# Kernel tuning notes

Hardware: AMD Instinct MI355X
Metric: run time of the kernel (lower is better)

The kernel has to match this reference:

```python
import jax, jax.numpy as jnp
import numpy as np

HEADS = 16
DIM_HEAD = 64
QUERY_DIM = 1024
INNER_DIM = HEADS * DIM_HEAD  # 1024
SCALE = DIM_HEAD ** (-0.5)


def setup_inputs() -> dict:
    key = jax.random.key(0)
    ks = jax.random.split(key, 6)
    B, S = 4, 2048
    hidden_states = jax.random.normal(ks[0], (B, S, QUERY_DIM), dtype=jnp.float32)
    # Linear weights stored as [in, out] for x @ W convention
    init = 1.0 / np.sqrt(QUERY_DIM)
    Wq = jax.random.uniform(ks[1], (QUERY_DIM, INNER_DIM), jnp.float32, -init, init)
    Wk = jax.random.uniform(ks[2], (QUERY_DIM, INNER_DIM), jnp.float32, -init, init)
    Wv = jax.random.uniform(ks[3], (QUERY_DIM, INNER_DIM), jnp.float32, -init, init)
    Wo = jax.random.uniform(ks[4], (INNER_DIM, QUERY_DIM), jnp.float32, -init, init)
    bo = jax.random.uniform(ks[5], (QUERY_DIM,), jnp.float32, -init, init)
    return {"hidden_states": hidden_states, "Wq": Wq, "Wk": Wk, "Wv": Wv, "Wo": Wo, "bo": bo}


def reference(hidden_states, Wq, Wk, Wv, Wo, bo):
    B, S, _ = hidden_states.shape
    # Projections
    q = hidden_states @ Wq  # [B,S,inner]
    k = hidden_states @ Wk
    v = hidden_states @ Wv
    # [B, H, S, D]
    q = q.reshape(B, S, HEADS, DIM_HEAD).transpose(0, 2, 1, 3)
    k = k.reshape(B, S, HEADS, DIM_HEAD).transpose(0, 2, 1, 3)
    v = v.reshape(B, S, HEADS, DIM_HEAD).transpose(0, 2, 1, 3)
    # Attention scores and softmax (scale after matmul, as in source)
    scores = jnp.einsum('bhqd,bhkd->bhqk', q, k) * SCALE
    attn = jax.nn.softmax(scores, axis=-1)
    out = jnp.einsum('bhqk,bhkd->bhqd', attn, v)  # [B,H,S,D]
    out = out.transpose(0, 2, 1, 3).reshape(B, S, INNER_DIM)
    return out @ Wo + bo
```

## Files before the change

kernel.cpp:

```cpp
#include <hip/hip_runtime.h>
#include <stdint.h>

typedef short v8s __attribute__((ext_vector_type(8)));
typedef float v4f __attribute__((ext_vector_type(4)));
typedef unsigned int u32;
typedef unsigned short us;

#define LOG2E 1.44269504088896340736f

__device__ __forceinline__ u32 f2u(float x) {
  union { float f; u32 u; } t; t.f = x; return t.u;
}

__device__ __forceinline__ unsigned short bfr(float x) {
  u32 u = f2u(x);
  u32 r = u + 0x7FFFu + ((u >> 16) & 1u);
  return (unsigned short)(r >> 16);
}

__device__ __forceinline__ u32 pk2(float a, float b) {
  return __builtin_amdgcn_perm(f2u(b) + 0x8000u, f2u(a) + 0x8000u, 0x07060302u);
}

__device__ __forceinline__ void async16(const void* g, void* l) {
  __builtin_amdgcn_global_load_lds(
      (const __attribute__((address_space(1))) u32*)g,
      (__attribute__((address_space(3))) u32*)l, 16, 0, 0);
}

#define MFMA_K32(A, B, C) __builtin_amdgcn_mfma_f32_16x16x32_bf16((A), (B), (C), 0, 0, 0)

__global__ __launch_bounds__(256)
void prologue_kernel(const float4* __restrict__ Hs, ushort4* __restrict__ Hb,
                     const float* __restrict__ W0, const float* __restrict__ W1,
                     const float* __restrict__ W2, const float* __restrict__ W3,
                     us* __restrict__ O0, us* __restrict__ O1,
                     us* __restrict__ O2, us* __restrict__ O3) {
  __shared__ float tile[32][33];
  const int bid = blockIdx.x;
  if (bid < 8192) {
    int i = bid * 256 + threadIdx.x;
    float4 v = Hs[i];
    ushort4 o;
    o.x = bfr(v.x); o.y = bfr(v.y); o.z = bfr(v.z); o.w = bfr(v.w);
    Hb[i] = o;
  } else {
    const int b = bid - 8192;
    const int z = b >> 10;
    const int ti = b & 1023;
    const float* in = (z == 0) ? W0 : (z == 1) ? W1 : (z == 2) ? W2 : W3;
    us* out = (z == 0) ? O0 : (z == 1) ? O1 : (z == 2) ? O2 : O3;
    const float scale = (z == 0) ? 0.125f * LOG2E : 1.0f;
    const int N = 1024;
    int n0 = (ti & 31) * 32, k0 = (ti >> 5) * 32;
    int tx = threadIdx.x & 31, ty = threadIdx.x >> 5;
#pragma unroll
    for (int j = 0; j < 32; j += 8)
      tile[ty + j][tx] = in[(size_t)(k0 + ty + j) * N + n0 + tx];
    __syncthreads();
#pragma unroll
    for (int j = 0; j < 32; j += 8)
      out[(size_t)(n0 + ty + j) * 1024 + k0 + tx] = bfr(tile[tx][ty + j] * scale);
  }
}

template <int MODE>
__global__ __launch_bounds__(512, 2)
void gemm3_kernel(const us* __restrict__ A, const us* __restrict__ Bt,
                  us* __restrict__ dQ, us* __restrict__ dK, us* __restrict__ dV,
                  float* __restrict__ outF, const float* __restrict__ bias) {
  __shared__ __align__(16) us sm[73728];
  us* const AsB = sm;
  us* const BsB = sm + 3 * 8192;

  const int tid = threadIdx.x;
  const int wid = tid >> 6;
  const int lane = tid & 63;
  const int quad = lane >> 4;
  const int l16 = lane & 15;
  const int tile_m = blockIdx.y * 128;
  const int tile_n = blockIdx.x * 256;
  const bool vpath = (MODE == 3) && (tile_n >= 2048);

  const int srow = tid >> 3;
  const int sc = tid & 7;
  const int scg = sc ^ (srow & 7);

  const us* const GA = A + (size_t)(tile_m + srow) * 1024 + scg * 8;
  const us* const GB = Bt + (size_t)(tile_n + srow) * 1024 + scg * 8;
  us* const LA = AsB + srow * 64 + sc * 8;
  us* const LB = BsB + srow * 64 + sc * 8;

  auto ISSUE = [&](int j, int b) {
    const us* ga = GA + j * 64;
    us* la = LA + b * 8192;
#pragma unroll
    for (int it = 0; it < 2; ++it)
      async16(ga + it * 64 * 1024, la + it * 64 * 64);
    const us* gb = GB + j * 64;
    us* lb = LB + b * 16384;
#pragma unroll
    for (int it = 0; it < 4; ++it)
      async16(gb + it * 64 * 1024, lb + it * 64 * 64);
  };

  v4f zero = {0.f, 0.f, 0.f, 0.f};
  v4f acc[4][4];
#pragma unroll
  for (int i = 0; i < 4; ++i)
#pragma unroll
    for (int j = 0; j < 4; ++j) acc[i][j] = zero;

  const int wm = (wid >> 2) * 64;
  const int wn = (wid & 3) * 64;

  ISSUE(0, 0);
  ISSUE(1, 1);

  int bt = 0;
#pragma unroll 1
  for (int t = 0; t < 16; ++t) {
    if (t < 15)
      asm volatile("s_waitcnt vmcnt(6)" ::: "memory");
    else
      asm volatile("s_waitcnt vmcnt(0)" ::: "memory");
    __builtin_amdgcn_s_barrier();
    asm volatile("" ::: "memory");

    if (t + 2 < 16) {
      int b2 = bt + 2;
      if (b2 >= 3) b2 -= 3;
      ISSUE(t + 2, b2);
    }

    const us* As = AsB + bt * 8192;
    const us* Bs = BsB + bt * 16384;
#pragma unroll
    for (int ks = 0; ks < 2; ++ks) {
      v8s a[4], b[4];
#pragma unroll
      for (int i = 0; i < 4; ++i) {
        int row = wm + i * 16 + l16;
        a[i] = *(const v8s*)&As[row * 64 + (((ks * 4 + quad) ^ (row & 7)) * 8)];
      }
#pragma unroll
      for (int j = 0; j < 4; ++j) {
        int row = wn + j * 16 + l16;
        b[j] = *(const v8s*)&Bs[row * 64 + (((ks * 4 + quad) ^ (row & 7)) * 8)];
      }
      __builtin_amdgcn_s_setprio(1);
      if (vpath) {
#pragma unroll
        for (int i = 0; i < 4; ++i)
#pragma unroll
          for (int j = 0; j < 4; ++j)
            acc[i][j] = MFMA_K32(a[i], b[j], acc[i][j]);
      } else {
#pragma unroll
        for (int i = 0; i < 4; ++i)
#pragma unroll
          for (int j = 0; j < 4; ++j)
            acc[i][j] = MFMA_K32(b[j], a[i], acc[i][j]);
      }
      __builtin_amdgcn_s_setprio(0);
    }
    if (++bt >= 3) bt = 0;
  }

  if (MODE == 2) {
#pragma unroll
    for (int i = 0; i < 4; ++i) {
      int row = tile_m + wm + i * 16 + l16;
#pragma unroll
      for (int j = 0; j < 4; ++j) {
        int col = tile_n + wn + j * 16 + quad * 4;
        float4 bv = *(const float4*)&bias[col];
        float4 o;
        o.x = acc[i][j][0] + bv.x; o.y = acc[i][j][1] + bv.y;
        o.z = acc[i][j][2] + bv.z; o.w = acc[i][j][3] + bv.w;
        *(float4*)&outF[(size_t)row * 1024 + col] = o;
      }
    }
  } else if (!vpath) {
    us* base = (tile_n < 1024) ? dQ : dK;
    const int coln = tile_n & 1023;
#pragma unroll
    for (int i = 0; i < 4; ++i) {
      int row = tile_m + wm + i * 16 + l16;
      int b_ = row >> 11, s_ = row & 2047;
#pragma unroll
      for (int j = 0; j < 4; ++j) {
        int col = coln + wn + j * 16 + quad * 4;
        int h = (col >> 6) & 15, d = col & 63;
        uint2 pk = make_uint2(pk2(acc[i][j][0], acc[i][j][1]), pk2(acc[i][j][2], acc[i][j][3]));
        *(uint2*)&base[((size_t)(b_ * 16 + h) * 2048 + s_) * 64 + d] = pk;
      }
    }
  } else {
    __syncthreads();
    const int vn = tile_n - 2048;
#pragma unroll
    for (int i = 0; i < 4; ++i) {
      int sp = wm + (i >> 1) * 32 + quad * 8 + (i & 1) * 4;
#pragma unroll
      for (int j = 0; j < 4; ++j) {
        int col = wn + j * 16 + l16;
        uint2 pk = make_uint2(pk2(acc[i][j][0], acc[i][j][1]), pk2(acc[i][j][2], acc[i][j][3]));
        *(uint2*)&sm[col * 132 + sp] = pk;
      }
    }
    __syncthreads();
    const int b_ = tile_m >> 11;
    const int sbase = tile_m & 2047;
#pragma unroll
    for (int it = 0; it < 8; ++it) {
      int u = it * 512 + tid;
      int col = u >> 4, sp = (u & 15) * 8;
      v8s val = *(const v8s*)&sm[col * 132 + sp];
      int colg = vn + col;
      int h = (colg >> 6) & 15, d = colg & 63;
      *(v8s*)&dV[((size_t)(b_ * 16 + h) * 64 + d) * 2048 + sbase + sp] = val;
    }
  }
}

__global__ __launch_bounds__(256, 2)
void flash_kernel(const us* __restrict__ Q, const us* __restrict__ K,
                  const us* __restrict__ Vt, us* __restrict__ O) {
  __shared__ __align__(16) us sm[32768];

  const int tid = threadIdx.x;
  const int wid = tid >> 6;
  const int lane = tid & 63;
  const int quad = lane >> 4;
  const int l16 = lane & 15;
  const int id = blockIdx.x;
  const int bh = id & 63;
  const int q0 = (id >> 6) * 256;
  const int wq = wid * 64;
  const us* Qp = Q + (size_t)bh * (2048 * 64);
  const us* Kp = K + (size_t)bh * (2048 * 64);
  const us* Vp = Vt + (size_t)bh * (64 * 2048);

  v8s qB[4][2];
#pragma unroll
  for (int mi = 0; mi < 4; ++mi)
#pragma unroll
    for (int ks = 0; ks < 2; ++ks)
      qB[mi][ks] = *(const v8s*)&Qp[(size_t)(q0 + wq + mi * 16 + l16) * 64 + ks * 32 + quad * 8];

  v4f zero = {0.f, 0.f, 0.f, 0.f};
  v4f o[4][4];
#pragma unroll
  for (int i = 0; i < 4; ++i)
#pragma unroll
    for (int mi = 0; mi < 4; ++mi) o[i][mi] = zero;
  v4f l_acc[4] = {zero, zero, zero, zero};
  const us one_bf = 0x3F80;
  const v8s ones = {(short)one_bf, (short)one_bf, (short)one_bf, (short)one_bf,
                    (short)one_bf, (short)one_bf, (short)one_bf, (short)one_bf};

  auto STAGE = [&](int kv0, int p) {
    us* Ks = sm + p * 16384;
    us* Vts = Ks + 8192;
    {
      int r0 = wid * 32 + (lane >> 3);
      int c = lane & 7;
#pragma unroll
      for (int it = 0; it < 4; ++it) {
        int rr = r0 + it * 8;
        int cg = c ^ (rr & 7);
        async16(Kp + (size_t)(kv0 + rr) * 64 + cg * 8, &Ks[rr * 64 + c * 8]);
      }
    }
    {
      int d0 = wid * 16 + (lane >> 4);
      int c = lane & 15;
#pragma unroll
      for (int it = 0; it < 4; ++it) {
        int dd = d0 + it * 4;
        int cg = c ^ (dd & 15);
        async16(Vp + (size_t)dd * 2048 + kv0 + cg * 8, &Vts[dd * 128 + c * 8]);
      }
    }
  };

  STAGE(0, 0);
  int buf = 0;
#pragma unroll 1
  for (int t = 0; t < 16; ++t) {
    asm volatile("s_waitcnt vmcnt(0)" ::: "memory");
    __builtin_amdgcn_s_barrier();
    asm volatile("" ::: "memory");
    if (t < 15) STAGE((t + 1) * 128, buf ^ 1);

    const us* Ks = sm + buf * 16384;
    const us* Vts = Ks + 8192;

#pragma unroll
    for (int hf = 0; hf < 2; ++hf) {
      v4f sT[4][4];
#pragma unroll
      for (int m = 0; m < 4; ++m)
#pragma unroll
        for (int mi = 0; mi < 4; ++mi) sT[m][mi] = zero;
#pragma unroll
      for (int ks = 0; ks < 2; ++ks) {
        v8s kA[4];
#pragma unroll
        for (int m = 0; m < 4; ++m) {
          int kvr = hf * 64 + m * 16 + l16;
          int cc = (ks * 4 + quad) ^ (l16 & 7);
          kA[m] = *(const v8s*)&Ks[kvr * 64 + cc * 8];
        }
#pragma unroll
        for (int m = 0; m < 4; ++m)
#pragma unroll
          for (int mi = 0; mi < 4; ++mi)
            sT[m][mi] = MFMA_K32(kA[m], qB[mi][ks], sT[m][mi]);
      }

#pragma unroll
      for (int cp = 0; cp < 2; ++cp) {
        v8s bp[4];
#pragma unroll
        for (int mi = 0; mi < 4; ++mi) {
          union { u32 w[4]; v8s s; } u;
#pragma unroll
          for (int dm = 0; dm < 2; ++dm) {
            int m = cp * 2 + dm;
            float p0 = __builtin_amdgcn_exp2f(sT[m][mi][0]);
            float p1 = __builtin_amdgcn_exp2f(sT[m][mi][1]);
            float p2 = __builtin_amdgcn_exp2f(sT[m][mi][2]);
            float p3 = __builtin_amdgcn_exp2f(sT[m][mi][3]);
            u.w[dm * 2] = pk2(p0, p1);
            u.w[dm * 2 + 1] = pk2(p2, p3);
          }
          bp[mi] = u.s;
          l_acc[mi] = MFMA_K32(ones, bp[mi], l_acc[mi]);
        }
#pragma unroll
        for (int i = 0; i < 4; ++i) {
          int d = i * 16 + l16;
          int cc = (hf * 8 + cp * 4 + quad) ^ (d & 15);
          v8s vt = *(const v8s*)&Vts[d * 128 + cc * 8];
#pragma unroll
          for (int mi = 0; mi < 4; ++mi)
            o[i][mi] = MFMA_K32(vt, bp[mi], o[i][mi]);
        }
      }
    }
    buf ^= 1;
  }

  float invl[4];
#pragma unroll
  for (int mi = 0; mi < 4; ++mi) invl[mi] = 1.0f / l_acc[mi][0];

  __syncthreads();
#pragma unroll
  for (int mi = 0; mi < 4; ++mi) {
    int q = wq + mi * 16 + l16;
#pragma unroll
    for (int i = 0; i < 4; ++i)
#pragma unroll
      for (int rp = 0; rp < 4; rp += 2) {
        int d = i * 16 + quad * 4 + rp;
        u32 pk = pk2(o[i][mi][rp] * invl[mi], o[i][mi][rp + 1] * invl[mi]);
        *(u32*)&sm[q * 64 + ((d >> 3) ^ (q & 7)) * 8 + (d & 7)] = pk;
      }
  }
  __syncthreads();
  const int b_ = bh >> 4, h_ = bh & 15;
#pragma unroll
  for (int it = 0; it < 8; ++it) {
    int u = it * 256 + tid;
    int row = u >> 3, ch = u & 7;
    v8s val = *(const v8s*)&sm[row * 64 + (ch ^ (row & 7)) * 8];
    *(v8s*)&O[((size_t)(b_ * 2048 + q0 + row)) * 1024 + h_ * 64 + ch * 8] = val;
  }
}

extern "C" void kernel_launch(void* const* d_in, const int* in_sizes, int n_in,
                              void* d_out, int out_size, void* d_ws, size_t ws_size,
                              hipStream_t stream) {
  const float* Hs = (const float*)d_in[0];
  const float* Wq = (const float*)d_in[1];
  const float* Wk = (const float*)d_in[2];
  const float* Wv = (const float*)d_in[3];
  const float* Wo = (const float*)d_in[4];
  const float* bo = (const float*)d_in[5];
  float* out = (float*)d_out;
  char* ws = (char*)d_ws;
  const size_t MiB = 1ull << 20;
  us* Hb  = (us*)(ws);
  us* Wqt = (us*)(ws + 16 * MiB);
  us* Wkt = (us*)(ws + 18 * MiB);
  us* Wvt = (us*)(ws + 20 * MiB);
  us* Wot = (us*)(ws + 22 * MiB);
  us* Qb  = (us*)(ws + 24 * MiB);
  us* Kb  = (us*)(ws + 40 * MiB);
  us* Vtb = (us*)(ws + 56 * MiB);
  us* Ob  = Hb;
  (void)Wkt; (void)Wvt;

  prologue_kernel<<<12288, 256, 0, stream>>>((const float4*)Hs, (ushort4*)Hb,
                                             Wq, Wk, Wv, Wo, Wqt, Wkt, Wvt, Wot);
  gemm3_kernel<3><<<dim3(12, 64), 512, 0, stream>>>(Hb, Wqt, Qb, Kb, Vtb, nullptr, nullptr);
  flash_kernel<<<512, 256, 0, stream>>>(Qb, Kb, Vtb, Ob);
  gemm3_kernel<2><<<dim3(4, 64), 512, 0, stream>>>(Ob, Wot, nullptr, nullptr, nullptr, out, bo);
}
```

Before: 259.4 us.

## Fuse fp32-to-bf16 activation cast into QKV GEMM A-tile loads

Removes the separate pass that converts hidden_states to bf16. The QKV GEMM now reads fp32 A tiles straight from global memory into registers, packs them to bf16 and writes them to LDS one stage ahead, while the B tiles keep using async global-to-LDS loads. This drops one full-activation write and read round trip. In exchange the A loads are register-staged, and each tile fetches twice the bytes from global memory. Launch bounds also change to 4 waves per SIMD, which may limit registers and cause spills.

```diff
diff --git a/kernel.cpp b/kernel.cpp
--- a/kernel.cpp
+++ b/kernel.cpp
@@ -30,45 +30,30 @@
 
 #define MFMA_K32(A, B, C) __builtin_amdgcn_mfma_f32_16x16x32_bf16((A), (B), (C), 0, 0, 0)
 
-__global__ __launch_bounds__(256)
-void prologue_kernel(const float4* __restrict__ Hs, ushort4* __restrict__ Hb,
-                     const float* __restrict__ W0, const float* __restrict__ W1,
-                     const float* __restrict__ W2, const float* __restrict__ W3,
-                     us* __restrict__ O0, us* __restrict__ O1,
-                     us* __restrict__ O2, us* __restrict__ O3) {
+__global__ void transpose_cast4_kernel(const float* __restrict__ W0, const float* __restrict__ W1,
+                                       const float* __restrict__ W2, const float* __restrict__ W3,
+                                       us* __restrict__ O0, us* __restrict__ O1,
+                                       us* __restrict__ O2, us* __restrict__ O3) {
   __shared__ float tile[32][33];
-  const int bid = blockIdx.x;
-  if (bid < 8192) {
-    int i = bid * 256 + threadIdx.x;
-    float4 v = Hs[i];
-    ushort4 o;
-    o.x = bfr(v.x); o.y = bfr(v.y); o.z = bfr(v.z); o.w = bfr(v.w);
-    Hb[i] = o;
-  } else {
-    const int b = bid - 8192;
-    const int z = b >> 10;
-    const int ti = b & 1023;
-    const float* in = (z == 0) ? W0 : (z == 1) ? W1 : (z == 2) ? W2 : W3;
-    us* out = (z == 0) ? O0 : (z == 1) ? O1 : (z == 2) ? O2 : O3;
-    const float scale = (z == 0) ? 0.125f * LOG2E : 1.0f;
-    const int N = 1024;
-    int n0 = (ti & 31) * 32, k0 = (ti >> 5) * 32;
-    int tx = threadIdx.x & 31, ty = threadIdx.x >> 5;
-#pragma unroll
-    for (int j = 0; j < 32; j += 8)
-      tile[ty + j][tx] = in[(size_t)(k0 + ty + j) * N + n0 + tx];
-    __syncthreads();
-#pragma unroll
-    for (int j = 0; j < 32; j += 8)
-      out[(size_t)(n0 + ty + j) * 1024 + k0 + tx] = bfr(tile[tx][ty + j] * scale);
-  }
-}
-
-template <int MODE>
-__global__ __launch_bounds__(512, 2)
-void gemm3_kernel(const us* __restrict__ A, const us* __restrict__ Bt,
-                  us* __restrict__ dQ, us* __restrict__ dK, us* __restrict__ dV,
-                  float* __restrict__ outF, const float* __restrict__ bias) {
+  const int z = blockIdx.z;
+  const float* in = (z == 0) ? W0 : (z == 1) ? W1 : (z == 2) ? W2 : W3;
+  us* out = (z == 0) ? O0 : (z == 1) ? O1 : (z == 2) ? O2 : O3;
+  const float scale = (z == 0) ? 0.125f * LOG2E : 1.0f;
+  const int N = 1024;
+  int n0 = blockIdx.x * 32, k0 = blockIdx.y * 32;
+  int tx = threadIdx.x, ty = threadIdx.y;
+#pragma unroll
+  for (int j = 0; j < 32; j += 8)
+    tile[ty + j][tx] = in[(size_t)(k0 + ty + j) * N + n0 + tx];
+  __syncthreads();
+#pragma unroll
+  for (int j = 0; j < 32; j += 8)
+    out[(size_t)(n0 + ty + j) * 1024 + k0 + tx] = bfr(tile[tx][ty + j] * scale);
+}
+
+__global__ __launch_bounds__(512, 4)
+void gemm_qkv_kernel(const float* __restrict__ A, const us* __restrict__ Bt,
+                     us* __restrict__ dQ, us* __restrict__ dK, us* __restrict__ dV) {
   __shared__ __align__(16) us sm[73728];
   us* const AsB = sm;
   us* const BsB = sm + 3 * 8192;
@@ -80,7 +65,167 @@
   const int l16 = lane & 15;
   const int tile_m = blockIdx.y * 128;
   const int tile_n = blockIdx.x * 256;
-  const bool vpath = (MODE == 3) && (tile_n >= 2048);
+  const bool vpath = (tile_n >= 2048);
+
+  const int srow = tid >> 3;
+  const int sc = tid & 7;
+  const int scg = sc ^ (srow & 7);
+
+  const float* const GA = A + (size_t)(tile_m + srow) * 1024 + scg * 8;
+  const us* const GB = Bt + (size_t)(tile_n + srow) * 1024 + scg * 8;
+  us* const LA = AsB + srow * 64 + sc * 8;
+  us* const LB = BsB + srow * 64 + sc * 8;
+
+  float4 aR[4];
+
+  auto LOAD_A = [&](int j) {
+    const float4* p0 = (const float4*)(GA + j * 64);
+    const float4* p1 = (const float4*)(GA + j * 64 + (size_t)64 * 1024);
+    aR[0] = p0[0]; aR[1] = p0[1];
+    aR[2] = p1[0]; aR[3] = p1[1];
+  };
+  auto WRITE_A = [&](int b) {
+    uint4 w0, w1;
+    w0.x = pk2(aR[0].x, aR[0].y); w0.y = pk2(aR[0].z, aR[0].w);
+    w0.z = pk2(aR[1].x, aR[1].y); w0.w = pk2(aR[1].z, aR[1].w);
+    w1.x = pk2(aR[2].x, aR[2].y); w1.y = pk2(aR[2].z, aR[2].w);
+    w1.z = pk2(aR[3].x, aR[3].y); w1.w = pk2(aR[3].z, aR[3].w);
+    *(uint4*)(LA + b * 8192) = w0;
+    *(uint4*)(LA + b * 8192 + 64 * 64) = w1;
+  };
+  auto ISSUE_B = [&](int j, int b) {
+    const us* gb = GB + j * 64;
+    us* lb = LB + b * 16384;
+#pragma unroll
+    for (int it = 0; it < 4; ++it)
+      async16(gb + it * 64 * 1024, lb + it * 64 * 64);
+  };
+
+  v4f zero = {0.f, 0.f, 0.f, 0.f};
+  v4f acc[4][4];
+#pragma unroll
+  for (int i = 0; i < 4; ++i)
+#pragma unroll
+    for (int j = 0; j < 4; ++j) acc[i][j] = zero;
+
+  const int wm = (wid >> 2) * 64;
+  const int wn = (wid & 3) * 64;
+
+  LOAD_A(0);
+  ISSUE_B(0, 0);
+  WRITE_A(0);
+  LOAD_A(1);
+  ISSUE_B(1, 1);
+
+  int bt = 0;
+#pragma unroll 1
+  for (int t = 0; t < 16; ++t) {
+    if (t < 15)
+      asm volatile("s_waitcnt vmcnt(8)" ::: "memory");
+    else
+      asm volatile("s_waitcnt vmcnt(0)" ::: "memory");
+    asm volatile("s_waitcnt lgkmcnt(0)" ::: "memory");
+    __builtin_amdgcn_s_barrier();
+    asm volatile("" ::: "memory");
+
+    {
+      int b1 = bt + 1; if (b1 >= 3) b1 -= 3;
+      int b2 = bt + 2; if (b2 >= 3) b2 -= 3;
+      if (t + 1 < 16) WRITE_A(b1);
+      if (t + 2 < 16) { LOAD_A(t + 2); ISSUE_B(t + 2, b2); }
+    }
+
+    const us* As = AsB + bt * 8192;
+    const us* Bs = BsB + bt * 16384;
+#pragma unroll
+    for (int ks = 0; ks < 2; ++ks) {
+      v8s a[4], b[4];
+#pragma unroll
+      for (int i = 0; i < 4; ++i) {
+        int row = wm + i * 16 + l16;
+        a[i] = *(const v8s*)&As[row * 64 + (((ks * 4 + quad) ^ (row & 7)) * 8)];
+      }
+#pragma unroll
+      for (int j = 0; j < 4; ++j) {
+        int row = wn + j * 16 + l16;
+        b[j] = *(const v8s*)&Bs[row * 64 + (((ks * 4 + quad) ^ (row & 7)) * 8)];
+      }
+      __builtin_amdgcn_s_setprio(1);
+      if (vpath) {
+#pragma unroll
+        for (int i = 0; i < 4; ++i)
+#pragma unroll
+          for (int j = 0; j < 4; ++j)
+            acc[i][j] = MFMA_K32(a[i], b[j], acc[i][j]);
+      } else {
+#pragma unroll
+        for (int i = 0; i < 4; ++i)
+#pragma unroll
+          for (int j = 0; j < 4; ++j)
+            acc[i][j] = MFMA_K32(b[j], a[i], acc[i][j]);
+      }
+      __builtin_amdgcn_s_setprio(0);
+    }
+    if (++bt >= 3) bt = 0;
+  }
+
+  if (!vpath) {
+    us* base = (tile_n < 1024) ? dQ : dK;
+    const int coln = tile_n & 1023;
+#pragma unroll
+    for (int i = 0; i < 4; ++i) {
+      int row = tile_m + wm + i * 16 + l16;
+      int b_ = row >> 11, s_ = row & 2047;
+#pragma unroll
+      for (int j = 0; j < 4; ++j) {
+        int col = coln + wn + j * 16 + quad * 4;
+        int h = (col >> 6) & 15, d = col & 63;
+        uint2 pk = make_uint2(pk2(acc[i][j][0], acc[i][j][1]), pk2(acc[i][j][2], acc[i][j][3]));
+        *(uint2*)&base[((size_t)(b_ * 16 + h) * 2048 + s_) * 64 + d] = pk;
+      }
+    }
+  } else {
+    __syncthreads();
+    const int vn = tile_n - 2048;
+#pragma unroll
+    for (int i = 0; i < 4; ++i) {
+      int sp = wm + (i >> 1) * 32 + quad * 8 + (i & 1) * 4;
+#pragma unroll
+      for (int j = 0; j < 4; ++j) {
+        int col = wn + j * 16 + l16;
+        uint2 pk = make_uint2(pk2(acc[i][j][0], acc[i][j][1]), pk2(acc[i][j][2], acc[i][j][3]));
+        *(uint2*)&sm[col * 132 + sp] = pk;
+      }
+    }
+    __syncthreads();
+    const int b_ = tile_m >> 11;
+    const int sbase = tile_m & 2047;
+#pragma unroll
+    for (int it = 0; it < 8; ++it) {
+      int u = it * 512 + tid;
+      int col = u >> 4, sp = (u & 15) * 8;
+      v8s val = *(const v8s*)&sm[col * 132 + sp];
+      int colg = vn + col;
+      int h = (colg >> 6) & 15, d = colg & 63;
+      *(v8s*)&dV[((size_t)(b_ * 16 + h) * 64 + d) * 2048 + sbase + sp] = val;
+    }
+  }
+}
+
+__global__ __launch_bounds__(512, 2)
+void gemm_out_kernel(const us* __restrict__ A, const us* __restrict__ Bt,
+                     float* __restrict__ outF, const float* __restrict__ bias) {
+  __shared__ __align__(16) us sm[73728];
+  us* const AsB = sm;
+  us* const BsB = sm + 3 * 8192;
+
+  const int tid = threadIdx.x;
+  const int wid = tid >> 6;
+  const int lane = tid & 63;
+  const int quad = lane >> 4;
+  const int l16 = lane & 15;
+  const int tile_m = blockIdx.y * 128;
+  const int tile_n = blockIdx.x * 256;
 
   const int srow = tid >> 3;
   const int sc = tid & 7;
@@ -149,77 +294,27 @@
         b[j] = *(const v8s*)&Bs[row * 64 + (((ks * 4 + quad) ^ (row & 7)) * 8)];
       }
       __builtin_amdgcn_s_setprio(1);
-      if (vpath) {
-#pragma unroll
-        for (int i = 0; i < 4; ++i)
-#pragma unroll
-          for (int j = 0; j < 4; ++j)
-            acc[i][j] = MFMA_K32(a[i], b[j], acc[i][j]);
-      } else {
-#pragma unroll
-        for (int i = 0; i < 4; ++i)
-#pragma unroll
-          for (int j = 0; j < 4; ++j)
-            acc[i][j] = MFMA_K32(b[j], a[i], acc[i][j]);
-      }
+#pragma unroll
+      for (int i = 0; i < 4; ++i)
+#pragma unroll
+        for (int j = 0; j < 4; ++j)
+          acc[i][j] = MFMA_K32(b[j], a[i], acc[i][j]);
       __builtin_amdgcn_s_setprio(0);
     }
     if (++bt >= 3) bt = 0;
   }
 
-  if (MODE == 2) {
-#pragma unroll
-    for (int i = 0; i < 4; ++i) {
-      int row = tile_m + wm + i * 16 + l16;
-#pragma unroll
-      for (int j = 0; j < 4; ++j) {
-        int col = tile_n + wn + j * 16 + quad * 4;
-        float4 bv = *(const float4*)&bias[col];
-        float4 o;
-        o.x = acc[i][j][0] + bv.x; o.y = acc[i][j][1] + bv.y;
-        o.z = acc[i][j][2] + bv.z; o.w = acc[i][j][3] + bv.w;
-        *(float4*)&outF[(size_t)row * 1024 + col] = o;
-      }
-    }
-  } else if (!vpath) {
-    us* base = (tile_n < 1024) ? dQ : dK;
-    const int coln = tile_n & 1023;
-#pragma unroll
-    for (int i = 0; i < 4; ++i) {
-      int row = tile_m + wm + i * 16 + l16;
-      int b_ = row >> 11, s_ = row & 2047;
-#pragma unroll
-      for (int j = 0; j < 4; ++j) {
-        int col = coln + wn + j * 16 + quad * 4;
-        int h = (col >> 6) & 15, d = col & 63;
-        uint2 pk = make_uint2(pk2(acc[i][j][0], acc[i][j][1]), pk2(acc[i][j][2], acc[i][j][3]));
-        *(uint2*)&base[((size_t)(b_ * 16 + h) * 2048 + s_) * 64 + d] = pk;
-      }
-    }
-  } else {
-    __syncthreads();
-    const int vn = tile_n - 2048;
-#pragma unroll
-    for (int i = 0; i < 4; ++i) {
-      int sp = wm + (i >> 1) * 32 + quad * 8 + (i & 1) * 4;
-#pragma unroll
-      for (int j = 0; j < 4; ++j) {
-        int col = wn + j * 16 + l16;
-        uint2 pk = make_uint2(pk2(acc[i][j][0], acc[i][j][1]), pk2(acc[i][j][2], acc[i][j][3]));
-        *(uint2*)&sm[col * 132 + sp] = pk;
-      }
-    }
-    __syncthreads();
-    const int b_ = tile_m >> 11;
-    const int sbase = tile_m & 2047;
-#pragma unroll
-    for (int it = 0; it < 8; ++it) {
-      int u = it * 512 + tid;
-      int col = u >> 4, sp = (u & 15) * 8;
-      v8s val = *(const v8s*)&sm[col * 132 + sp];
-      int colg = vn + col;
-      int h = (colg >> 6) & 15, d = colg & 63;
-      *(v8s*)&dV[((size_t)(b_ * 16 + h) * 64 + d) * 2048 + sbase + sp] = val;
+#pragma unroll
+  for (int i = 0; i < 4; ++i) {
+    int row = tile_m + wm + i * 16 + l16;
+#pragma unroll
+    for (int j = 0; j < 4; ++j) {
+      int col = tile_n + wn + j * 16 + quad * 4;
+      float4 bv = *(const float4*)&bias[col];
+      float4 o;
+      o.x = acc[i][j][0] + bv.x; o.y = acc[i][j][1] + bv.y;
+      o.z = acc[i][j][2] + bv.z; o.w = acc[i][j][3] + bv.w;
+      *(float4*)&outF[(size_t)row * 1024 + col] = o;
     }
   }
 }
@@ -393,7 +488,7 @@
   float* out = (float*)d_out;
   char* ws = (char*)d_ws;
   const size_t MiB = 1ull << 20;
-  us* Hb  = (us*)(ws);
+  us* Ob  = (us*)(ws);
   us* Wqt = (us*)(ws + 16 * MiB);
   us* Wkt = (us*)(ws + 18 * MiB);
   us* Wvt = (us*)(ws + 20 * MiB);
@@ -401,12 +496,11 @@
   us* Qb  = (us*)(ws + 24 * MiB);
   us* Kb  = (us*)(ws + 40 * MiB);
   us* Vtb = (us*)(ws + 56 * MiB);
-  us* Ob  = Hb;
   (void)Wkt; (void)Wvt;
 
-  prologue_kernel<<<12288, 256, 0, stream>>>((const float4*)Hs, (ushort4*)Hb,
-                                             Wq, Wk, Wv, Wo, Wqt, Wkt, Wvt, Wot);
-  gemm3_kernel<3><<<dim3(12, 64), 512, 0, stream>>>(Hb, Wqt, Qb, Kb, Vtb, nullptr, nullptr);
+  transpose_cast4_kernel<<<dim3(32, 32, 4), dim3(32, 8), 0, stream>>>(Wq, Wk, Wv, Wo,
+                                                                      Wqt, Wkt, Wvt, Wot);
+  gemm_qkv_kernel<<<dim3(12, 64), 512, 0, stream>>>(Hs, Wqt, Qb, Kb, Vtb);
   flash_kernel<<<512, 256, 0, stream>>>(Qb, Kb, Vtb, Ob);
-  gemm3_kernel<2><<<dim3(4, 64), 512, 0, stream>>>(Ob, Wot, nullptr, nullptr, nullptr, out, bo);
-}
+  gemm_out_kernel<<<dim3(4, 64), 512, 0, stream>>>(Ob, Wot, out, bo);
+}
```

Result: no change. 258.6 us (-0.3%).
